# Kernel tuning notes

Measured on AMD Instinct MI355X. Metric: run time of the kernel, lower is better.

## Reference

```python
import jax, jax.numpy as jnp
import numpy as np

DIM = 32
DEPTH = 2  # closed-form Lyndon-basis log-signature implemented for depth 2


def setup_inputs() -> dict:
    key = jax.random.key(0)
    B, L, D = 512, 2048, DIM
    x = jax.random.normal(key, (B, L, D), dtype=jnp.float32)
    return {"x": x}


def _logsig_depth2(x):
    # x: (B, L, D) batch of paths.
    dx = x[:, 1:, :] - x[:, :-1, :]                     # (B, L-1, D) increments
    prefix = jnp.cumsum(dx, axis=1)                      # inclusive prefix sums
    level1 = prefix[:, -1, :]                            # (B, D) total displacement
    prefix_excl = prefix - dx                            # prefix up to t-1 (exclusive)
    # level-2 signature S_ij = sum_t prefix_excl[t, i] * dx[t, j]  -> (B, D, D)
    S2 = jnp.einsum("bli,blj->bij", prefix_excl, dx)
    # log-signature level 2 = antisymmetric part (Levy areas), Lyndon words i<j
    A = 0.5 * (S2 - jnp.swapaxes(S2, 1, 2))             # (B, D, D)
    iu, ju = jnp.triu_indices(x.shape[-1], k=1)          # row-major upper triangle
    areas = A[:, iu, ju]                                 # (B, D*(D-1)/2)
    return jnp.concatenate([level1, areas], axis=-1)     # (B, D + D*(D-1)/2)


def reference(x):
    # Faithful batched equivalent of iisignature.logsig(path, prepare(dim, 2))
    # for every path in the batch (Lyndon basis, depth 2).
    return _logsig_depth2(x)
```

## Files before the change

kernel.cpp:

```cpp
#include <hip/hip_runtime.h>
#include <stdint.h>


constexpr int kB   = 512;
constexpr int kL   = 2048;
constexpr int kD   = 32;
constexpr int kOut = 528;
constexpr int kPan = 32;
constexpr int kTw  = 128;
constexpr int kNP  = kTw / kPan;

typedef __attribute__((ext_vector_type(8))) short bfrag;
typedef __attribute__((ext_vector_type(4))) float f4acc;
union FragU { uint32_t u[4]; bfrag f; };

__global__ __launch_bounds__(256, 8)
void logsig_mfma(const float* __restrict__ x, float* __restrict__ out) {
    __shared__ float sW[4][kD * kD];
    __shared__ float sx0[kD], sL1[kD];

    const int b     = blockIdx.x >> 2;
    const int chunk = blockIdx.x & 3;
    const int tid   = threadIdx.x;
    const int wave  = tid >> 6;
    const int lane  = tid & 63;
    const int m     = lane & 15;
    const int q     = lane >> 4;

    const float* __restrict__ xb = x + (size_t)b * (kL * kD);
    const int t0  = chunk * (4 * kTw) + wave * kTw;
    const int rb0 = t0 + q * 8;

    const uint32_t* __restrict__ base =
        (const uint32_t*)xb + (size_t)rb0 * kD + m;

    f4acc acc[4];
    #pragma unroll
    for (int t = 0; t < 4; ++t)
        #pragma unroll
        for (int e = 0; e < 4; ++e) acc[t][e] = 0.0f;

    auto load_panel = [&](int p, uint32_t* e0, uint32_t* e1) {
        const uint32_t* bp = base + (size_t)p * kPan * kD;
        #pragma unroll
        for (int j = 0; j < 8; ++j) {
            e0[j] = bp[j * kD];
            e1[j] = bp[j * kD + 16];
        }
        const int rb = rb0 + p * kPan;
        const int ex = (rb + 8 <= kL - 1 ? 8 : (kL - 1) - rb) * kD;
        e0[8] = bp[ex];
        e1[8] = bp[ex + 16];
    };

    auto make_frags = [&](const uint32_t* e, FragU& AH, FragU& AL,
                          FragU& BH, FragU& BL) {
        uint32_t l[9];
        #pragma unroll
        for (int j = 0; j < 9; ++j) {
            const uint32_t fh = e[j] & 0xffff0000u;
            const float r = __builtin_bit_cast(float, e[j])
                          - __builtin_bit_cast(float, fh);
            l[j] = __builtin_bit_cast(uint32_t, r);
        }
        #pragma unroll
        for (int d = 0; d < 4; ++d) {
            AH.u[d] = __builtin_amdgcn_perm(e[2*d+1], e[2*d],   0x07060302u);
            AL.u[d] = __builtin_amdgcn_perm(l[2*d+1], l[2*d],   0x07060302u);
            BH.u[d] = __builtin_amdgcn_perm(e[2*d+2], e[2*d+1], 0x07060302u);
            BL.u[d] = __builtin_amdgcn_perm(l[2*d+2], l[2*d+1], 0x07060302u);
        }
    };

    uint32_t buf[2][2][9];
    load_panel(0, buf[0][0], buf[0][1]);

    #pragma unroll
    for (int p = 0; p < kNP; ++p) {
        const int cu = p & 1, nx = cu ^ 1;
        if (p + 1 < kNP) load_panel(p + 1, buf[nx][0], buf[nx][1]);

        FragU A0H, A0L, B0H, B0L, A1H, A1L, B1H, B1L;
        make_frags(buf[cu][0], A0H, A0L, B0H, B0L);
        make_frags(buf[cu][1], A1H, A1L, B1H, B1L);

        acc[0] = __builtin_amdgcn_mfma_f32_16x16x32_bf16(A0H.f, B0H.f, acc[0], 0, 0, 0);
        acc[0] = __builtin_amdgcn_mfma_f32_16x16x32_bf16(A0H.f, B0L.f, acc[0], 0, 0, 0);
        acc[0] = __builtin_amdgcn_mfma_f32_16x16x32_bf16(A0L.f, B0H.f, acc[0], 0, 0, 0);
        acc[1] = __builtin_amdgcn_mfma_f32_16x16x32_bf16(A0H.f, B1H.f, acc[1], 0, 0, 0);
        acc[1] = __builtin_amdgcn_mfma_f32_16x16x32_bf16(A0H.f, B1L.f, acc[1], 0, 0, 0);
        acc[1] = __builtin_amdgcn_mfma_f32_16x16x32_bf16(A0L.f, B1H.f, acc[1], 0, 0, 0);
        acc[2] = __builtin_amdgcn_mfma_f32_16x16x32_bf16(A1H.f, B0H.f, acc[2], 0, 0, 0);
        acc[2] = __builtin_amdgcn_mfma_f32_16x16x32_bf16(A1H.f, B0L.f, acc[2], 0, 0, 0);
        acc[2] = __builtin_amdgcn_mfma_f32_16x16x32_bf16(A1L.f, B0H.f, acc[2], 0, 0, 0);
        acc[3] = __builtin_amdgcn_mfma_f32_16x16x32_bf16(A1H.f, B1H.f, acc[3], 0, 0, 0);
        acc[3] = __builtin_amdgcn_mfma_f32_16x16x32_bf16(A1H.f, B1L.f, acc[3], 0, 0, 0);
        acc[3] = __builtin_amdgcn_mfma_f32_16x16x32_bf16(A1L.f, B1H.f, acc[3], 0, 0, 0);
    }

    #pragma unroll
    for (int t = 0; t < 4; ++t) {
        const int tr = t >> 1, tc = t & 1;
        #pragma unroll
        for (int e = 0; e < 4; ++e) {
            const int row = 16 * tr + q * 4 + e;
            const int col = 16 * tc + m;
            sW[wave][row * kD + col] = acc[t][e];
        }
    }
    if (tid < kD) {
        const float x0v = xb[tid];
        const float xev = xb[(size_t)(kL - 1) * kD + tid];
        sx0[tid] = x0v;
        sL1[tid] = xev - x0v;
    }
    __syncthreads();

    for (int c = tid; c < kD * kD; c += 256)
        sW[0][c] += sW[1][c] + sW[2][c] + sW[3][c];
    __syncthreads();

    float* ob = out + (size_t)b * kOut;
    for (int o = tid; o < kOut; o += 256) {
        if (o < 32) {
            if (chunk == 0) ob[o] = sL1[o];
        } else {
            int p = o - 32, i = 0;
            while (p >= 31 - i) { p -= 31 - i; ++i; }
            const int j = i + 1 + p;
            float v = 0.5f * (sW[0][i * kD + j] - sW[0][j * kD + i]);
            if (chunk == 0)
                v += 0.5f * (sx0[j] * sL1[i] - sx0[i] * sL1[j]);
            atomicAdd(ob + o, v);
        }
    }
}

extern "C" void kernel_launch(void* const* d_in, const int* in_sizes, int n_in,
                              void* d_out, int out_size, void* d_ws, size_t ws_size,
                              hipStream_t stream) {
    const float* x = (const float*)d_in[0];
    float* out = (float*)d_out;
    hipMemsetAsync(out, 0, (size_t)out_size * sizeof(float), stream);
    logsig_mfma<<<dim3(kB * 4), dim3(256), 0, stream>>>(x, out);
}
```

Measured before the change: 197.4 us.

## Stage input panels into LDS with async global_load_lds double buffering

Replaces the per-lane strided global loads of each 32-row panel with coalesced 16-byte loads that go straight into a per-wave double-buffered LDS staging area, using global_load_lds when the builtin is available. Fragments are then read from LDS. The one halo row that crosses a panel boundary is fetched from global memory separately, and explicit vmcnt waits order the loads. Each wave now covers 256 timesteps instead of 128, so the grid is halved, launch bounds drop to 4 blocks per CU, and the staging buffers are reused for the final reduction. The aim is better coalescing and load/MFMA overlap; the cost is fewer blocks to hide latency and reliance on hand-written waitcnt ordering.

```diff
diff --git a/kernel.cpp b/kernel.cpp
--- a/kernel.cpp
+++ b/kernel.cpp
@@ -2,25 +2,33 @@
 #include <stdint.h>
 
 
-constexpr int kB   = 512;
-constexpr int kL   = 2048;
-constexpr int kD   = 32;
-constexpr int kOut = 528;
-constexpr int kPan = 32;
-constexpr int kTw  = 128;
-constexpr int kNP  = kTw / kPan;
+constexpr int kB    = 512;
+constexpr int kL    = 2048;
+constexpr int kD    = 32;
+constexpr int kOut  = 528;
+constexpr int kPan  = 32;
+constexpr int kTw   = 256;
+constexpr int kNP   = kTw / kPan;
+constexpr int kCS   = 264;
+constexpr int kBuf  = 4 * kCS;
 
 typedef __attribute__((ext_vector_type(8))) short bfrag;
 typedef __attribute__((ext_vector_type(4))) float f4acc;
 union FragU { uint32_t u[4]; bfrag f; };
 
-__global__ __launch_bounds__(256, 8)
+#if defined(__has_builtin)
+#if __has_builtin(__builtin_amdgcn_global_load_lds)
+#define LOGSIG_ASYNC_LDS 1
+#endif
+#endif
+
+__global__ __launch_bounds__(256, 4)
 void logsig_mfma(const float* __restrict__ x, float* __restrict__ out) {
-    __shared__ float sW[4][kD * kD];
+    __shared__ __align__(16) uint32_t sStage[4][2][kBuf];
     __shared__ float sx0[kD], sL1[kD];
 
-    const int b     = blockIdx.x >> 2;
-    const int chunk = blockIdx.x & 3;
+    const int b     = blockIdx.x >> 1;
+    const int chunk = blockIdx.x & 1;
     const int tid   = threadIdx.x;
     const int wave  = tid >> 6;
     const int lane  = tid & 63;
@@ -28,30 +36,33 @@
     const int q     = lane >> 4;
 
     const float* __restrict__ xb = x + (size_t)b * (kL * kD);
-    const int t0  = chunk * (4 * kTw) + wave * kTw;
-    const int rb0 = t0 + q * 8;
+    const int t0w = chunk * 1024 + wave * kTw;
 
-    const uint32_t* __restrict__ base =
-        (const uint32_t*)xb + (size_t)rb0 * kD + m;
+    auto stage_panel = [&](int p, int nb) {
+        uint32_t* dst = &sStage[wave][nb][0];
+        const uint32_t* src = (const uint32_t*)xb + (size_t)(t0w + p * kPan) * kD;
+        #pragma unroll
+        for (int c = 0; c < 4; ++c) {
+            const uint32_t* g = src + c * 256 + lane * 4;
+            uint32_t* l = dst + c * kCS;
+#ifdef LOGSIG_ASYNC_LDS
+            auto* gp = reinterpret_cast<const __attribute__((address_space(1))) uint32_t*>(
+                reinterpret_cast<uintptr_t>(g));
+            auto* lp = reinterpret_cast<__attribute__((address_space(3))) uint32_t*>(
+                reinterpret_cast<uintptr_t>(l));
+            __builtin_amdgcn_global_load_lds(gp, lp, 16, 0, 0);
+#else
+            const float4 v = *(const float4*)g;
+            *(float4*)(l + lane * 4) = v;
+#endif
+        }
+    };
 
     f4acc acc[4];
     #pragma unroll
     for (int t = 0; t < 4; ++t)
         #pragma unroll
         for (int e = 0; e < 4; ++e) acc[t][e] = 0.0f;
-
-    auto load_panel = [&](int p, uint32_t* e0, uint32_t* e1) {
-        const uint32_t* bp = base + (size_t)p * kPan * kD;
-        #pragma unroll
-        for (int j = 0; j < 8; ++j) {
-            e0[j] = bp[j * kD];
-            e1[j] = bp[j * kD + 16];
-        }
-        const int rb = rb0 + p * kPan;
-        const int ex = (rb + 8 <= kL - 1 ? 8 : (kL - 1) - rb) * kD;
-        e0[8] = bp[ex];
-        e1[8] = bp[ex + 16];
-    };
 
     auto make_frags = [&](const uint32_t* e, FragU& AH, FragU& AL,
                           FragU& BH, FragU& BL) {
@@ -72,17 +83,46 @@
         }
     };
 
-    uint32_t buf[2][2][9];
-    load_panel(0, buf[0][0], buf[0][1]);
+    stage_panel(0, 0);
 
-    #pragma unroll
+    #pragma unroll 2
     for (int p = 0; p < kNP; ++p) {
-        const int cu = p & 1, nx = cu ^ 1;
-        if (p + 1 < kNP) load_panel(p + 1, buf[nx][0], buf[nx][1]);
+        const int cu = p & 1, nb = cu ^ 1;
+
+        uint32_t h0 = 0, h1 = 0;
+        if (q == 3) {
+            int hr = t0w + p * kPan + 32;
+            hr = hr < kL - 1 ? hr : kL - 1;
+            const uint32_t* g = (const uint32_t*)xb + (size_t)hr * kD + m;
+            h0 = g[0];
+            h1 = g[16];
+        }
+
+        if (p + 1 < kNP) {
+            stage_panel(p + 1, nb);
+            asm volatile("s_waitcnt vmcnt(4)" ::: "memory");
+        } else {
+            asm volatile("s_waitcnt vmcnt(0)" ::: "memory");
+        }
+
+        const uint32_t* sb = &sStage[wave][cu][0];
+        uint32_t e0[9], e1[9];
+        #pragma unroll
+        for (int j = 0; j < 8; ++j) {
+            const int a = q * kCS + j * 32 + m;
+            e0[j] = sb[a];
+            e1[j] = sb[a + 16];
+        }
+        {
+            const int a = (q < 3 ? (q + 1) * kCS + m : 3 * kCS + 7 * 32 + m);
+            const uint32_t d0 = sb[a], d1 = sb[a + 16];
+            e0[8] = (q < 3) ? d0 : h0;
+            e1[8] = (q < 3) ? d1 : h1;
+        }
 
         FragU A0H, A0L, B0H, B0L, A1H, A1L, B1H, B1L;
-        make_frags(buf[cu][0], A0H, A0L, B0H, B0L);
-        make_frags(buf[cu][1], A1H, A1L, B1H, B1L);
+        make_frags(e0, A0H, A0L, B0H, B0L);
+        make_frags(e1, A1H, A1L, B1H, B1L);
 
         acc[0] = __builtin_amdgcn_mfma_f32_16x16x32_bf16(A0H.f, B0H.f, acc[0], 0, 0, 0);
         acc[0] = __builtin_amdgcn_mfma_f32_16x16x32_bf16(A0H.f, B0L.f, acc[0], 0, 0, 0);
@@ -98,6 +138,7 @@
         acc[3] = __builtin_amdgcn_mfma_f32_16x16x32_bf16(A1L.f, B1H.f, acc[3], 0, 0, 0);
     }
 
+    float* sWw = (float*)&sStage[wave][0][0];
     #pragma unroll
     for (int t = 0; t < 4; ++t) {
         const int tr = t >> 1, tc = t & 1;
@@ -105,7 +146,7 @@
         for (int e = 0; e < 4; ++e) {
             const int row = 16 * tr + q * 4 + e;
             const int col = 16 * tc + m;
-            sW[wave][row * kD + col] = acc[t][e];
+            sWw[row * kD + col] = acc[t][e];
         }
     }
     if (tid < kD) {
@@ -116,8 +157,11 @@
     }
     __syncthreads();
 
+    float* sW0 = (float*)&sStage[0][0][0];
     for (int c = tid; c < kD * kD; c += 256)
-        sW[0][c] += sW[1][c] + sW[2][c] + sW[3][c];
+        sW0[c] += ((float*)&sStage[1][0][0])[c]
+                + ((float*)&sStage[2][0][0])[c]
+                + ((float*)&sStage[3][0][0])[c];
     __syncthreads();
 
     float* ob = out + (size_t)b * kOut;
@@ -128,7 +172,7 @@
             int p = o - 32, i = 0;
             while (p >= 31 - i) { p -= 31 - i; ++i; }
             const int j = i + 1 + p;
-            float v = 0.5f * (sW[0][i * kD + j] - sW[0][j * kD + i]);
+            float v = 0.5f * (sW0[i * kD + j] - sW0[j * kD + i]);
             if (chunk == 0)
                 v += 0.5f * (sx0[j] * sL1[i] - sx0[i] * sL1[j]);
             atomicAdd(ob + o, v);
@@ -142,5 +186,5 @@
     const float* x = (const float*)d_in[0];
     float* out = (float*)d_out;
     hipMemsetAsync(out, 0, (size_t)out_size * sizeof(float), stream);
-    logsig_mfma<<<dim3(kB * 4), dim3(256), 0, stream>>>(x, out);
+    logsig_mfma<<<dim3(kB * 2), dim3(256), 0, stream>>>(x, out);
 }
```

New measurement: 191.8 us. 1.03x faster.
